# Performance work log

Measured on AMD Instinct MI355X. Metric: run time of the kernel, lower is better.

Reference implementation:

```python
import jax, jax.numpy as jnp
import numpy as np

EPS = 1e-06

def feature_map(x):
    # elu(x) + 1
    return jax.nn.elu(x) + 1.0

def setup_inputs() -> dict:
    key = jax.random.key(0)
    kq, kk, kv = jax.random.split(key, 3)
    N, L, S, H, D = 8, 8192, 8192, 8, 32
    queries = jax.random.normal(kq, (N, L, H, D), dtype=jnp.float32)
    keys = jax.random.normal(kk, (N, S, H, D), dtype=jnp.float32)
    values = jax.random.normal(kv, (N, S, H, D), dtype=jnp.float32)
    return {"queries": queries, "keys": keys, "values": values}

def reference(queries, keys, values):
    # Linear attention ("Transformers are RNNs"), faithful to forward_linear.
    Q = feature_map(queries)          # [N, L, H, D]
    K = feature_map(keys)             # [N, S, H, D]
    v_length = values.shape[1]
    vals = values / v_length          # [N, S, H, Dv]
    KV = jnp.einsum('nshd,nshv->nhdv', K, vals)            # [N, H, D, Dv]
    Z = 1.0 / (jnp.einsum('nlhd,nhd->nlh', Q, K.sum(axis=1)) + EPS)  # [N, L, H]
    out = jnp.einsum('nlhd,nhdv,nlh->nlhv', Q, KV, Z) * v_length     # [N, L, H, Dv]
    return out
```

## Files before the change

kernel.cpp:

```cpp
#include <hip/hip_runtime.h>


#define L_Q 8192
#define S_K 8192
#define DIM 32
#define RS 256
#define EPSV 1e-6f
#define NPAIR 64
#define WSFLOATS (NPAIR * 1056)

__device__ __forceinline__ float fmap(float x) {
    return x > 0.0f ? x + 1.0f : __expf(x);
}

#define CHUNKS 32
#define SROWS (S_K / CHUNKS)
#define A_ITERS (SROWS / 32)
#define SKP 36

union SmemA {
    struct { float K[4][8][SKP]; float V[4][8][SKP]; } st;
    struct { float red[4][64][16]; float redk[4][32]; } rd;
};

__global__ __launch_bounds__(256, 5) void kv_kernel(const float* __restrict__ Kg,
                                                    const float* __restrict__ Vg,
                                                    float* __restrict__ ws)
{
    __shared__ SmemA sm;
    const int pair = blockIdx.y;
    const int n = pair >> 3, h = pair & 7;
    const int t = threadIdx.x;
    const int w = t >> 6;
    const int l = t & 63;
    const int g = l >> 4;
    const int i = l & 15;
    const int db = i >> 2;
    const int vb = i & 3;

    const int srow = l >> 3;
    const int scol = (l & 7) * 4;

    const size_t base = ((size_t)n * S_K + (size_t)blockIdx.x * SROWS) * RS
                      + (size_t)h * DIM;
    size_t gaddr = base + (size_t)(w * 8 + srow) * RS + scol;

    float acc[8][8];
    float ksum[8];
    #pragma unroll
    for (int a = 0; a < 8; ++a) {
        ksum[a] = 0.0f;
        #pragma unroll
        for (int b = 0; b < 8; ++b) acc[a][b] = 0.0f;
    }

    float4 pK = *(const float4*)(Kg + gaddr);
    float4 pV = *(const float4*)(Vg + gaddr);

    float (*sK)[SKP] = sm.st.K[w];
    float (*sV)[SKP] = sm.st.V[w];

    for (int it = 0; it < A_ITERS; ++it) {
        float4 a = pK;
        a.x = fmap(a.x); a.y = fmap(a.y); a.z = fmap(a.z); a.w = fmap(a.w);
        *(float4*)(&sK[srow][scol]) = a;
        *(float4*)(&sV[srow][scol]) = pV;
        if (it + 1 < A_ITERS) {
            gaddr += (size_t)32 * RS;
            pK = *(const float4*)(Kg + gaddr);
            pV = *(const float4*)(Vg + gaddr);
        }
        #pragma unroll
        for (int rr = 0; rr < 2; ++rr) {
            const int r = 2 * g + rr;
            const float4 k0 = *(const float4*)&sK[r][db * 8];
            const float4 k1 = *(const float4*)&sK[r][db * 8 + 4];
            const float4 v0 = *(const float4*)&sV[r][vb * 8];
            const float4 v1 = *(const float4*)&sV[r][vb * 8 + 4];
            const float kk[8] = {k0.x,k0.y,k0.z,k0.w,k1.x,k1.y,k1.z,k1.w};
            const float vv[8] = {v0.x,v0.y,v0.z,v0.w,v1.x,v1.y,v1.z,v1.w};
            #pragma unroll
            for (int a2 = 0; a2 < 8; ++a2) {
                ksum[a2] += kk[a2];
                #pragma unroll
                for (int b2 = 0; b2 < 8; ++b2) acc[a2][b2] += kk[a2] * vv[b2];
            }
        }
    }

    #pragma unroll
    for (int a = 0; a < 8; ++a) {
        #pragma unroll
        for (int b = 0; b < 8; ++b) {
            acc[a][b] += __shfl_xor(acc[a][b], 16);
            acc[a][b] += __shfl_xor(acc[a][b], 32);
        }
        ksum[a] += __shfl_xor(ksum[a], 16);
        ksum[a] += __shfl_xor(ksum[a], 32);
    }
    __syncthreads();
    if (l < 16) {
        #pragma unroll
        for (int a = 0; a < 8; ++a)
            #pragma unroll
            for (int b = 0; b < 8; ++b)
                sm.rd.red[w][a * 8 + b][i] = acc[a][b];
        if (vb == 0) {
            #pragma unroll
            for (int a = 0; a < 8; ++a) sm.rd.redk[w][db * 8 + a] = ksum[a];
        }
    }
    __syncthreads();
    float* KVp = ws + pair * 1056;
    #pragma unroll
    for (int p = t; p < 1024; p += 256) {
        const int kIdx = p >> 4, iIdx = p & 15;
        const float v = sm.rd.red[0][kIdx][iIdx] + sm.rd.red[1][kIdx][iIdx]
                      + sm.rd.red[2][kIdx][iIdx] + sm.rd.red[3][kIdx][iIdx];
        const int d  = ((iIdx >> 2) << 3) + (kIdx >> 3);
        const int vv = ((iIdx & 3) << 3) + (kIdx & 7);
        unsafeAtomicAdd(&KVp[d * DIM + vv], v);
    }
    if (t < 32) {
        const float v = sm.rd.redk[0][t] + sm.rd.redk[1][t]
                      + sm.rd.redk[2][t] + sm.rd.redk[3][t];
        unsafeAtomicAdd(&KVp[1024 + t], v);
    }
}

#define BROWS 128
#define TP 132

__global__ __launch_bounds__(256, 8) void out_kernel(const float* __restrict__ Q,
                                                     const float* __restrict__ ws,
                                                     float* __restrict__ out)
{
    __shared__ float sQt[DIM][TP];
    __shared__ float sKV[DIM][DIM];
    __shared__ float sKs[DIM];

    const int pair = blockIdx.y;
    const int n = pair >> 3, h = pair & 7;
    const int t = threadIdx.x;
    const int w = t >> 6, l = t & 63;
    const int vb = l & 7;
    const int rb = l >> 3;

    const float* wp = ws + pair * 1056;
    for (int p = t; p < 1024; p += 256) (&sKV[0][0])[p] = wp[p];
    if (t < DIM) sKs[t] = wp[1024 + t];

    const size_t qbase = ((size_t)n * L_Q + (size_t)blockIdx.x * BROWS) * RS
                       + (size_t)h * DIM;

    {
        const int r = t >> 1;
        const int half = (t & 1) * 16;
        const float* qp = Q + qbase + (size_t)r * RS + half;
        #pragma unroll
        for (int j = 0; j < 4; ++j) {
            const float4 v = *(const float4*)(qp + j * 4);
            sQt[half + j * 4 + 0][r] = fmap(v.x);
            sQt[half + j * 4 + 1][r] = fmap(v.y);
            sQt[half + j * 4 + 2][r] = fmap(v.z);
            sQt[half + j * 4 + 3][r] = fmap(v.w);
        }
    }
    __syncthreads();

    const int rowbase = w * 32 + rb * 4;
    float acc[4][4];
    float den[4] = {0.0f, 0.0f, 0.0f, 0.0f};
    #pragma unroll
    for (int j = 0; j < 4; ++j)
        #pragma unroll
        for (int b = 0; b < 4; ++b) acc[j][b] = 0.0f;

    #pragma unroll
    for (int d = 0; d < DIM; ++d) {
        const float4 q4 = *(const float4*)&sQt[d][rowbase];
        const float ksd = sKs[d];
        const float4 c = *(const float4*)&sKV[d][vb * 4];
        const float qq[4] = {q4.x, q4.y, q4.z, q4.w};
        const float cc[4] = {c.x, c.y, c.z, c.w};
        #pragma unroll
        for (int j = 0; j < 4; ++j) {
            den[j] += qq[j] * ksd;
            #pragma unroll
            for (int b = 0; b < 4; ++b) acc[j][b] += qq[j] * cc[b];
        }
    }

    #pragma unroll
    for (int j = 0; j < 4; ++j) {
        const float z = 1.0f / (den[j] + EPSV);
        float4 o;
        o.x = acc[j][0] * z; o.y = acc[j][1] * z;
        o.z = acc[j][2] * z; o.w = acc[j][3] * z;
        *(float4*)(out + qbase + (size_t)(rowbase + j) * RS + vb * 4) = o;
    }
}

extern "C" void kernel_launch(void* const* d_in, const int* in_sizes, int n_in,
                              void* d_out, int out_size, void* d_ws, size_t ws_size,
                              hipStream_t stream)
{
    const float* Q = (const float*)d_in[0];
    const float* K = (const float*)d_in[1];
    const float* V = (const float*)d_in[2];
    float* outp = (float*)d_out;
    float* ws = (float*)d_ws;

    hipMemsetAsync(d_ws, 0, WSFLOATS * sizeof(float), stream);

    dim3 gA(CHUNKS, NPAIR);
    kv_kernel<<<gA, 256, 0, stream>>>(K, V, ws);

    dim3 gB(L_Q / BROWS, NPAIR);
    out_kernel<<<gB, 256, 0, stream>>>(Q, ws, outp);
}
```

Before: 274.4 us.

## Shrink per-thread KV tile and double chunk count in kv_kernel

Reworks the KV accumulation so each thread holds a 4x8 tile instead of 8x8, with two row-groups per wave instead of four, reducing register pressure and shuffle reductions. Chunk count along S doubles to launch more blocks, and the final reduction reads float4 from a re-laid-out shared buffer. Launch-bounds occupancy hints are dropped on both kernels. This adds more atomic adds into the workspace and lowers arithmetic intensity per shared-memory load.

```diff
diff --git a/kernel.cpp b/kernel.cpp
--- a/kernel.cpp
+++ b/kernel.cpp
@@ -13,19 +13,19 @@
     return x > 0.0f ? x + 1.0f : __expf(x);
 }
 
-#define CHUNKS 32
+#define CHUNKS 64
 #define SROWS (S_K / CHUNKS)
 #define A_ITERS (SROWS / 32)
 #define SKP 36
 
 union SmemA {
     struct { float K[4][8][SKP]; float V[4][8][SKP]; } st;
-    struct { float red[4][64][16]; float redk[4][32]; } rd;
+    struct { float red[4][32][36]; float redk[4][32]; } rd;
 };
 
-__global__ __launch_bounds__(256, 5) void kv_kernel(const float* __restrict__ Kg,
-                                                    const float* __restrict__ Vg,
-                                                    float* __restrict__ ws)
+__global__ __launch_bounds__(256) void kv_kernel(const float* __restrict__ Kg,
+                                                 const float* __restrict__ Vg,
+                                                 float* __restrict__ ws)
 {
     __shared__ SmemA sm;
     const int pair = blockIdx.y;
@@ -33,10 +33,10 @@
     const int t = threadIdx.x;
     const int w = t >> 6;
     const int l = t & 63;
-    const int g = l >> 4;
-    const int i = l & 15;
-    const int db = i >> 2;
-    const int vb = i & 3;
+    const int rsp = l >> 5;
+    const int q = l & 31;
+    const int d0 = (q >> 2) * 4;
+    const int v0 = (q & 3) * 8;
 
     const int srow = l >> 3;
     const int scol = (l & 7) * 4;
@@ -45,10 +45,10 @@
                       + (size_t)h * DIM;
     size_t gaddr = base + (size_t)(w * 8 + srow) * RS + scol;
 
-    float acc[8][8];
-    float ksum[8];
-    #pragma unroll
-    for (int a = 0; a < 8; ++a) {
+    float acc[4][8];
+    float ksum[4];
+    #pragma unroll
+    for (int a = 0; a < 4; ++a) {
         ksum[a] = 0.0f;
         #pragma unroll
         for (int b = 0; b < 8; ++b) acc[a][b] = 0.0f;
@@ -71,16 +71,15 @@
             pV = *(const float4*)(Vg + gaddr);
         }
         #pragma unroll
-        for (int rr = 0; rr < 2; ++rr) {
-            const int r = 2 * g + rr;
-            const float4 k0 = *(const float4*)&sK[r][db * 8];
-            const float4 k1 = *(const float4*)&sK[r][db * 8 + 4];
-            const float4 v0 = *(const float4*)&sV[r][vb * 8];
-            const float4 v1 = *(const float4*)&sV[r][vb * 8 + 4];
-            const float kk[8] = {k0.x,k0.y,k0.z,k0.w,k1.x,k1.y,k1.z,k1.w};
-            const float vv[8] = {v0.x,v0.y,v0.z,v0.w,v1.x,v1.y,v1.z,v1.w};
-            #pragma unroll
-            for (int a2 = 0; a2 < 8; ++a2) {
+        for (int rr = 0; rr < 4; ++rr) {
+            const int r = rsp * 4 + rr;
+            const float4 k4 = *(const float4*)&sK[r][d0];
+            const float4 va = *(const float4*)&sV[r][v0];
+            const float4 vb4 = *(const float4*)&sV[r][v0 + 4];
+            const float kk[4] = {k4.x, k4.y, k4.z, k4.w};
+            const float vv[8] = {va.x, va.y, va.z, va.w, vb4.x, vb4.y, vb4.z, vb4.w};
+            #pragma unroll
+            for (int a2 = 0; a2 < 4; ++a2) {
                 ksum[a2] += kk[a2];
                 #pragma unroll
                 for (int b2 = 0; b2 < 8; ++b2) acc[a2][b2] += kk[a2] * vv[b2];
@@ -89,51 +88,52 @@
     }
 
     #pragma unroll
-    for (int a = 0; a < 8; ++a) {
-        #pragma unroll
-        for (int b = 0; b < 8; ++b) {
-            acc[a][b] += __shfl_xor(acc[a][b], 16);
-            acc[a][b] += __shfl_xor(acc[a][b], 32);
-        }
-        ksum[a] += __shfl_xor(ksum[a], 16);
+    for (int a = 0; a < 4; ++a) {
         ksum[a] += __shfl_xor(ksum[a], 32);
+        #pragma unroll
+        for (int b = 0; b < 8; ++b) acc[a][b] += __shfl_xor(acc[a][b], 32);
     }
     __syncthreads();
-    if (l < 16) {
-        #pragma unroll
-        for (int a = 0; a < 8; ++a)
+    if (l < 32) {
+        #pragma unroll
+        for (int a = 0; a < 4; ++a)
             #pragma unroll
             for (int b = 0; b < 8; ++b)
-                sm.rd.red[w][a * 8 + b][i] = acc[a][b];
-        if (vb == 0) {
-            #pragma unroll
-            for (int a = 0; a < 8; ++a) sm.rd.redk[w][db * 8 + a] = ksum[a];
+                sm.rd.red[w][q][a * 8 + b] = acc[a][b];
+        if ((q & 3) == 0) {
+            #pragma unroll
+            for (int a = 0; a < 4; ++a) sm.rd.redk[w][q + a] = ksum[a];
         }
     }
     __syncthreads();
     float* KVp = ws + pair * 1056;
-    #pragma unroll
-    for (int p = t; p < 1024; p += 256) {
-        const int kIdx = p >> 4, iIdx = p & 15;
-        const float v = sm.rd.red[0][kIdx][iIdx] + sm.rd.red[1][kIdx][iIdx]
-                      + sm.rd.red[2][kIdx][iIdx] + sm.rd.red[3][kIdx][iIdx];
-        const int d  = ((iIdx >> 2) << 3) + (kIdx >> 3);
-        const int vv = ((iIdx & 3) << 3) + (kIdx & 7);
-        unsafeAtomicAdd(&KVp[d * DIM + vv], v);
+    {
+        const int d = t >> 3;
+        const int v = (t & 7) * 4;
+        const int lq = (d >> 2) * 4 + (v >> 3);
+        const int idx = (d & 3) * 8 + (v & 7);
+        const float4 s0 = *(const float4*)&sm.rd.red[0][lq][idx];
+        const float4 s1 = *(const float4*)&sm.rd.red[1][lq][idx];
+        const float4 s2 = *(const float4*)&sm.rd.red[2][lq][idx];
+        const float4 s3 = *(const float4*)&sm.rd.red[3][lq][idx];
+        unsafeAtomicAdd(&KVp[d * DIM + v + 0], s0.x + s1.x + s2.x + s3.x);
+        unsafeAtomicAdd(&KVp[d * DIM + v + 1], s0.y + s1.y + s2.y + s3.y);
+        unsafeAtomicAdd(&KVp[d * DIM + v + 2], s0.z + s1.z + s2.z + s3.z);
+        unsafeAtomicAdd(&KVp[d * DIM + v + 3], s0.w + s1.w + s2.w + s3.w);
     }
     if (t < 32) {
-        const float v = sm.rd.redk[0][t] + sm.rd.redk[1][t]
+        const float s = sm.rd.redk[0][t] + sm.rd.redk[1][t]
                       + sm.rd.redk[2][t] + sm.rd.redk[3][t];
-        unsafeAtomicAdd(&KVp[1024 + t], v);
+        unsafeAtomicAdd(&KVp[1024 + t], s);
     }
 }
 
 #define BROWS 128
 #define TP 132
 
-__global__ __launch_bounds__(256, 8) void out_kernel(const float* __restrict__ Q,
-                                                     const float* __restrict__ ws,
-                                                     float* __restrict__ out)
+__global__ __launch_bounds__(256) void out_kernel(const float* __restrict__ Q,
+                                                  const float* __restrict__ ws,
+                                                  float* __restrict__ out)
 {
     __shared__ float sQt[DIM][TP];
     __shared__ float sKV[DIM][DIM];
```

New measurement: 251.1 us. 1.09x faster.
